# Kernel optimization log

Measured on AMD Instinct MI355X. Metric: run time of the kernel, lower is better.

The kernel has to match this reference:

```python
import jax, jax.numpy as jnp
import numpy as np

E = 2048          # embed_size
H = 32            # nums_head
KVH = 8           # nums_kv_head
D = E // H        # head_dim = 64
G = H // KVH      # group size = 4


def setup_inputs() -> dict:
    key = jax.random.key(0)
    ks = jax.random.split(key, 9)
    s = 0.02
    return {
        "datas": jax.random.normal(ks[0], (2, 2048, E), dtype=jnp.float32),
        "Wq": jax.random.normal(ks[1], (E, E), dtype=jnp.float32) * s,
        "bq": jnp.zeros((E,), dtype=jnp.float32),
        "Wk": jax.random.normal(ks[2], (E, KVH * D), dtype=jnp.float32) * s,
        "bk": jnp.zeros((KVH * D,), dtype=jnp.float32),
        "Wv": jax.random.normal(ks[3], (E, KVH * D), dtype=jnp.float32) * s,
        "bv": jnp.zeros((KVH * D,), dtype=jnp.float32),
        "Wo": jax.random.normal(ks[4], (E, E), dtype=jnp.float32) * s,
        "bo": jnp.zeros((E,), dtype=jnp.float32),
    }


def reference(datas, Wq, bq, Wk, bk, Wv, bv, Wo, bo):
    B, S, _ = datas.shape
    q = (datas @ Wq + bq).reshape(B, S, H, D).transpose(0, 2, 1, 3)    # [B,H,S,D]
    k = (datas @ Wk + bk).reshape(B, S, KVH, D).transpose(0, 2, 1, 3)  # [B,KVH,S,D]
    v = (datas @ Wv + bv).reshape(B, S, KVH, D).transpose(0, 2, 1, 3)
    # repeat_interleave along head dim: each kv head serves G consecutive q heads
    k = jnp.repeat(k, G, axis=1)  # [B,H,S,D]
    v = jnp.repeat(v, G, axis=1)
    scores = jnp.einsum("bhqd,bhkd->bhqk", q, k) / jnp.sqrt(jnp.asarray(D, q.dtype))
    attn = jax.nn.softmax(scores, axis=-1)  # dropout = identity (eval)
    out = jnp.einsum("bhqk,bhkd->bhqd", attn, v)       # [B,H,S,D]
    out = out.transpose(0, 2, 1, 3).reshape(B, S, E)   # [B,S,E]
    return out @ Wo + bo
```

## Files before the change

### kernel.cpp

```cpp
#include <hip/hip_runtime.h>
#include <hip/hip_bf16.h>
#include <stdint.h>


#define S_LEN 2048
#define EMB   2048
#define NH    32
#define NKVH  8
#define HD    64
#define MTOT  4096
#define NQKV  3072
#define KDIM  2048
#define QSCALE 0.18033688011112042f

typedef __attribute__((ext_vector_type(8))) short short8;
typedef __attribute__((ext_vector_type(4))) float f32x4;
typedef __attribute__((ext_vector_type(4))) unsigned int u32x4;
typedef unsigned int u32;

__device__ __forceinline__ unsigned short f2bf(float x) {
    unsigned int u = __builtin_bit_cast(unsigned int, x);
    u = (u + 0x7FFFu + ((u >> 16) & 1u)) >> 16;
    return (unsigned short)u;
}

__device__ __forceinline__ u32 cvtpk_bf16(float a, float b) {
    u32 r;
    asm("v_cvt_pk_bf16_f32 %0, %1, %2" : "=v"(r) : "v"(a), "v"(b));
    return r;
}

__device__ __forceinline__ float exp2_raw(float x) {
#if __has_builtin(__builtin_amdgcn_exp2f)
    return __builtin_amdgcn_exp2f(x);
#else
    float r;
    asm("v_exp_f32 %0, %1" : "=v"(r) : "v"(x));
    return r;
#endif
}

__device__ __forceinline__ float rcp_raw(float x) {
#if __has_builtin(__builtin_amdgcn_rcpf)
    return __builtin_amdgcn_rcpf(x);
#else
    float r;
    asm("v_rcp_f32 %0, %1" : "=v"(r) : "v"(x));
    return r;
#endif
}

#define GLOAD(src, dst)                                                                   \
    __builtin_amdgcn_global_load_lds((const __attribute__((address_space(1))) void*)(src),\
                                     (__attribute__((address_space(3))) void*)(dst), 16, 0, 0)

__global__ void cvt_x(const float* __restrict__ x, unsigned short* __restrict__ o, int n4) {
    int stride = gridDim.x * blockDim.x;
    for (int i = blockIdx.x * blockDim.x + threadIdx.x; i < n4; i += stride) {
        float4 v = ((const float4*)x)[i];
        ushort4 r;
        r.x = f2bf(v.x); r.y = f2bf(v.y); r.z = f2bf(v.z); r.w = f2bf(v.w);
        ((ushort4*)o)[i] = r;
    }
}

__global__ void transpose_all(const float* __restrict__ Wq, const float* __restrict__ Wk,
                              const float* __restrict__ Wv, const float* __restrict__ Wo,
                              const float* __restrict__ bq, const float* __restrict__ bk,
                              const float* __restrict__ bv,
                              unsigned short* __restrict__ Wqkvt, unsigned short* __restrict__ Wot,
                              float* __restrict__ biasq) {
    const int x = blockIdx.x;
    if (x == 80) {
        if (blockIdx.y == 0)
            for (int i = threadIdx.x; i < NQKV; i += 256) {
                if (i < EMB) biasq[i] = bq[i] * QSCALE;
                else if (i < EMB + 512) biasq[i] = bk[i - EMB];
                else biasq[i] = bv[i - EMB - 512];
            }
        return;
    }
    const float* src; unsigned short* dst; int N, rowOfs, nt; float scale;
    if (x < 32)      { src = Wq; dst = Wqkvt; N = 2048; rowOfs = 0;    nt = x;      scale = QSCALE; }
    else if (x < 40) { src = Wk; dst = Wqkvt; N = 512;  rowOfs = 2048; nt = x - 32; scale = 1.0f; }
    else if (x < 48) { src = Wv; dst = Wqkvt; N = 512;  rowOfs = 2560; nt = x - 40; scale = 1.0f; }
    else             { src = Wo; dst = Wot;   N = 2048; rowOfs = 0;    nt = x - 48; scale = 1.0f; }

    __shared__ float t[64][65];
    int n0 = nt * 64, k0 = blockIdx.y * 64;
    int c = threadIdx.x & 63, r0 = threadIdx.x >> 6;
    #pragma unroll
    for (int r = r0; r < 64; r += 4) t[r][c] = src[(size_t)(k0 + r) * N + n0 + c];
    __syncthreads();
    #pragma unroll
    for (int r = r0; r < 64; r += 4)
        dst[(size_t)(rowOfs + n0 + r) * KDIM + k0 + c] = f2bf(t[c][r] * scale);
}

__global__ void transpose_v(const unsigned short* __restrict__ qkv, unsigned short* __restrict__ vt) {
    __shared__ unsigned short t[64][72];
    int s0 = blockIdx.x * 64; int kvh = blockIdx.y; int b = blockIdx.z;
    int c = threadIdx.x & 63, r0 = threadIdx.x >> 6;
    #pragma unroll
    for (int r = r0; r < 64; r += 4)
        t[r][c] = qkv[(size_t)(b * S_LEN + s0 + r) * NQKV + (EMB + NKVH * HD) + kvh * HD + c];
    __syncthreads();
    #pragma unroll
    for (int r = r0; r < 64; r += 4)
        vt[(size_t)((b * NKVH + kvh) * HD + r) * S_LEN + s0 + c] = t[c][r];
}

template <bool OUT_BF16>
__global__ __launch_bounds__(256) void gemm_bt(const unsigned short* __restrict__ A,
                                               const unsigned short* __restrict__ Bt,
                                               const float* __restrict__ bias,
                                               void* __restrict__ Cout, int N) {
    __shared__ __align__(16) unsigned short As[128 * 32];
    __shared__ __align__(16) unsigned short Bs[128 * 32];
    const int t = threadIdx.x;
    const int lane = t & 63;
    const int l15 = lane & 15, hi = lane >> 4;
    const int w = t >> 6;
    const int wm = (w >> 1) * 64, wn = (w & 1) * 64;

    const unsigned nbx = gridDim.x;
    const unsigned flat = blockIdx.y * nbx + blockIdx.x;
    const unsigned cpx = (nbx * gridDim.y) >> 3;
    const unsigned swz = (flat & 7u) * cpx + (flat >> 3);
    const int m0 = (int)(swz / nbx) * 128, n0 = (int)(swz % nbx) * 128;

    const int srow = t >> 2, scol = (t & 3) * 8;
    const unsigned short* ag0 = A + (size_t)(m0 + srow) * KDIM + scol;
    const unsigned short* ag1 = ag0 + (size_t)64 * KDIM;
    const unsigned short* bg0 = Bt + (size_t)(n0 + srow) * KDIM + scol;
    const unsigned short* bg1 = bg0 + (size_t)64 * KDIM;

    f32x4 acc[4][4] = {};

    for (int k0 = 0; k0 < KDIM; k0 += 32) {
        GLOAD(ag0 + k0, As + t * 8);
        GLOAD(ag1 + k0, As + 2048 + t * 8);
        GLOAD(bg0 + k0, Bs + t * 8);
        GLOAD(bg1 + k0, Bs + 2048 + t * 8);
        __syncthreads();
        short8 af[4], bf[4];
        #pragma unroll
        for (int m = 0; m < 4; m++)
            af[m] = *(const short8*)(As + (wm + m * 16 + l15) * 32 + hi * 8);
        #pragma unroll
        for (int n = 0; n < 4; n++)
            bf[n] = *(const short8*)(Bs + (wn + n * 16 + l15) * 32 + hi * 8);
        __builtin_amdgcn_s_setprio(1);
        #pragma unroll
        for (int m = 0; m < 4; m++)
            #pragma unroll
            for (int n = 0; n < 4; n++)
                acc[m][n] = __builtin_amdgcn_mfma_f32_16x16x32_bf16(af[m], bf[n], acc[m][n], 0, 0, 0);
        __builtin_amdgcn_s_setprio(0);
        __syncthreads();
    }

    #pragma unroll
    for (int m = 0; m < 4; m++) {
        int row = m0 + wm + m * 16 + hi * 4;
        #pragma unroll
        for (int n = 0; n < 4; n++) {
            int col = n0 + wn + n * 16 + l15;
            float bb = bias[col];
            #pragma unroll
            for (int i = 0; i < 4; i++) {
                float v = acc[m][n][i] + bb;
                if (OUT_BF16) ((unsigned short*)Cout)[(size_t)(row + i) * N + col] = f2bf(v);
                else          ((float*)Cout)[(size_t)(row + i) * N + col] = v;
            }
        }
    }
}

__global__ __launch_bounds__(512, 4) void attn(const unsigned short* __restrict__ qkv,
                                               const unsigned short* __restrict__ vt,
                                               unsigned short* __restrict__ out) {
    constexpr int NT = S_LEN / 64;
    const int qt = blockIdx.x, h = blockIdx.y, b = blockIdx.z;
    const int kvh = h >> 2;
    const int t = threadIdx.x, lane = t & 63, w = t >> 6;
    const int l15 = lane & 15, hi = lane >> 4;
    const int xsw = l15 & 7;

    __shared__ __align__(16) unsigned short Ks[2][64 * 64];
    __shared__ __align__(16) unsigned short Vs[2][64 * 64];

    const int grpA = ((hi & 1) << 1) | (hi >> 1);
    const int laneA = l15 + grpA * 16;
    const int laneB = laneA ^ 16;
    const bool top = hi >= 2;

    u32x4 onesw;
    onesw[0] = 0x3F803F80u; onesw[1] = 0x3F803F80u; onesw[2] = 0x3F803F80u; onesw[3] = 0x3F803F80u;
    const short8 ones = __builtin_bit_cast(short8, onesw);
    const f32x4 fzero = {};

    const int qrow0 = b * S_LEN + qt * 256 + w * 32;
    short8 qf[2][2];
    #pragma unroll
    for (int nt = 0; nt < 2; nt++)
        #pragma unroll
        for (int ks = 0; ks < 2; ks++)
            qf[nt][ks] = *(const short8*)(qkv + (size_t)(qrow0 + nt * 16 + l15) * NQKV + h * HD + ks * 32 + hi * 8);

    f32x4 o[4][2] = {};
    f32x4 osum[2] = {};

    const unsigned short* kbase = qkv + (size_t)b * S_LEN * NQKV + EMB + kvh * HD;
    const unsigned short* vbase = vt + (size_t)(b * NKVH + kvh) * HD * S_LEN;

    const int sr = t >> 3;
    const int sc16 = ((t & 7) ^ (sr & 7)) * 8;
    const unsigned short* kg0 = kbase + (size_t)sr * NQKV + sc16;
    const unsigned short* vg0 = vbase + (size_t)sr * S_LEN + sc16;

#define STAGE(buf, kv0)                                               \
    do {                                                              \
        GLOAD(kg0 + (size_t)(kv0) * NQKV, &Ks[buf][t * 8]);           \
        GLOAD(vg0 + (kv0),                &Vs[buf][t * 8]);           \
    } while (0)

    STAGE(0, 0);
    __syncthreads();

    for (int tt = 0; tt < NT; tt++) {
        const int cur = tt & 1;
        if (tt + 1 < NT) STAGE(cur ^ 1, (tt + 1) * 64);

        const unsigned short* Kc = Ks[cur];
        const unsigned short* Vc = Vs[cur];

        f32x4 sc[4][2];
        {
            short8 kf[4];
            #pragma unroll
            for (int mt = 0; mt < 4; mt++)
                kf[mt] = *(const short8*)(Kc + (mt * 16 + l15) * 64 + ((hi ^ xsw) * 8));
            __builtin_amdgcn_s_setprio(1);
            #pragma unroll
            for (int mt = 0; mt < 4; mt++)
                #pragma unroll
                for (int nt = 0; nt < 2; nt++)
                    sc[mt][nt] = __builtin_amdgcn_mfma_f32_16x16x32_bf16(kf[mt], qf[nt][0], fzero, 0, 0, 0);
            __builtin_amdgcn_s_setprio(0);
        }
        {
            short8 kf[4];
            #pragma unroll
            for (int mt = 0; mt < 4; mt++)
                kf[mt] = *(const short8*)(Kc + (mt * 16 + l15) * 64 + (((4 + hi) ^ xsw) * 8));
            __builtin_amdgcn_s_setprio(1);
            #pragma unroll
            for (int mt = 0; mt < 4; mt++)
                #pragma unroll
                for (int nt = 0; nt < 2; nt++)
                    sc[mt][nt] = __builtin_amdgcn_mfma_f32_16x16x32_bf16(kf[mt], qf[nt][1], sc[mt][nt], 0, 0, 0);
            __builtin_amdgcn_s_setprio(0);
        }

        u32 w0[4][2], w1[4][2];
        #pragma unroll
        for (int nt = 0; nt < 2; nt++)
            #pragma unroll
            for (int mt = 0; mt < 4; mt++) {
                #pragma unroll
                for (int i = 0; i < 4; i++)
                    sc[mt][nt][i] = exp2_raw(sc[mt][nt][i]);
                w0[mt][nt] = cvtpk_bf16(sc[mt][nt][0], sc[mt][nt][1]);
                w1[mt][nt] = cvtpk_bf16(sc[mt][nt][2], sc[mt][nt][3]);
            }

        #pragma unroll
        for (int ks = 0; ks < 2; ks++) {
            short8 vf[4];
            #pragma unroll
            for (int dt = 0; dt < 4; dt++)
                vf[dt] = *(const short8*)(Vc + (dt * 16 + l15) * 64 + (((ks * 4 + hi) ^ xsw) * 8));
            #pragma unroll
            for (int nt = 0; nt < 2; nt++) {
                u32 a0 = (hi & 1) ? w0[2 * ks + 1][nt] : w0[2 * ks][nt];
                u32 a1 = (hi & 1) ? w1[2 * ks + 1][nt] : w1[2 * ks][nt];
                u32 b0 = (hi & 1) ? w0[2 * ks][nt] : w0[2 * ks + 1][nt];
                u32 b1 = (hi & 1) ? w1[2 * ks][nt] : w1[2 * ks + 1][nt];
                u32 r0 = (u32)__shfl((int)a0, laneA);
                u32 r1 = (u32)__shfl((int)a1, laneA);
                u32 r2 = (u32)__shfl((int)b0, laneB);
                u32 r3 = (u32)__shfl((int)b1, laneB);
                u32x4 pw;
                pw[0] = top ? r2 : r0;
                pw[1] = top ? r3 : r1;
                pw[2] = top ? r0 : r2;
                pw[3] = top ? r1 : r3;
                short8 pa = __builtin_bit_cast(short8, pw);
                __builtin_amdgcn_s_setprio(1);
                osum[nt] = __builtin_amdgcn_mfma_f32_16x16x32_bf16(ones, pa, osum[nt], 0, 0, 0);
                #pragma unroll
                for (int dt = 0; dt < 4; dt++)
                    o[dt][nt] = __builtin_amdgcn_mfma_f32_16x16x32_bf16(vf[dt], pa, o[dt][nt], 0, 0, 0);
                __builtin_amdgcn_s_setprio(0);
            }
        }
        __syncthreads();
    }
#undef STAGE

    #pragma unroll
    for (int nt = 0; nt < 2; nt++) {
        float inv = rcp_raw(osum[nt][0]);
        size_t rbase = (size_t)(qrow0 + nt * 16 + l15) * EMB + h * HD;
        #pragma unroll
        for (int dt = 0; dt < 4; dt++) {
            uint2 pk;
            pk.x = cvtpk_bf16(o[dt][nt][0] * inv, o[dt][nt][1] * inv);
            pk.y = cvtpk_bf16(o[dt][nt][2] * inv, o[dt][nt][3] * inv);
            *(uint2*)(out + rbase + dt * 16 + hi * 4) = pk;
        }
    }
}

extern "C" void kernel_launch(void* const* d_in, const int* in_sizes, int n_in,
                              void* d_out, int out_size, void* d_ws, size_t ws_size,
                              hipStream_t stream) {
    const float* datas = (const float*)d_in[0];
    const float* Wq = (const float*)d_in[1];
    const float* bq = (const float*)d_in[2];
    const float* Wk = (const float*)d_in[3];
    const float* bk = (const float*)d_in[4];
    const float* Wv = (const float*)d_in[5];
    const float* bv = (const float*)d_in[6];
    const float* Wo = (const float*)d_in[7];
    const float* bo = (const float*)d_in[8];
    float* out = (float*)d_out;

    char* ws = (char*)d_ws;
    unsigned short* Xb = (unsigned short*)ws;      ws += (size_t)MTOT * KDIM * 2;
    unsigned short* Wqkvt = (unsigned short*)ws;   ws += (size_t)NQKV * KDIM * 2;
    unsigned short* Wot = (unsigned short*)ws;     ws += (size_t)EMB * KDIM * 2;
    float* biasq = (float*)ws;                     ws += (size_t)NQKV * 4;
    unsigned short* QKV = (unsigned short*)ws;     ws += (size_t)MTOT * NQKV * 2;
    unsigned short* Vt = (unsigned short*)ws;      ws += (size_t)2 * NKVH * HD * S_LEN * 2;
    unsigned short* AO = (unsigned short*)ws;      ws += (size_t)MTOT * EMB * 2;

    cvt_x<<<2048, 256, 0, stream>>>(datas, Xb, MTOT * KDIM / 4);
    transpose_all<<<dim3(81, 32), 256, 0, stream>>>(Wq, Wk, Wv, Wo, bq, bk, bv,
                                                    Wqkvt, Wot, biasq);

    gemm_bt<true><<<dim3(NQKV / 128, MTOT / 128), 256, 0, stream>>>(Xb, Wqkvt, biasq, QKV, NQKV);
    transpose_v<<<dim3(S_LEN / 64, NKVH, 2), 256, 0, stream>>>(QKV, Vt);
    attn<<<dim3(S_LEN / 256, NH, 2), 512, 0, stream>>>(QKV, Vt, AO);
    gemm_bt<false><<<dim3(EMB / 128, MTOT / 128), 256, 0, stream>>>(AO, Wot, bo, out, EMB);
}
```

Measured before the change: 226.1 us.

## Double GEMM K-tile to 64 with XOR-swizzled LDS layout

The bf16 GEMM now stages a 128x64 K-slab per iteration instead of 128x32, halving the number of barrier pairs and loop iterations. The LDS rows are stored with an XOR swizzle of the 16-byte chunk index by row, and the fragment reads apply the same swizzle, to avoid LDS bank conflicts on the wider rows. LDS use per block doubles to 32 KB, which may reduce occupancy.

Measured after the change: 213.4 us. 5.6% less time.

```diff
diff --git a/kernel.cpp b/kernel.cpp
--- a/kernel.cpp
+++ b/kernel.cpp
@@ -115,11 +115,12 @@
                                                const unsigned short* __restrict__ Bt,
                                                const float* __restrict__ bias,
                                                void* __restrict__ Cout, int N) {
-    __shared__ __align__(16) unsigned short As[128 * 32];
-    __shared__ __align__(16) unsigned short Bs[128 * 32];
+    __shared__ __align__(16) unsigned short As[128 * 64];
+    __shared__ __align__(16) unsigned short Bs[128 * 64];
     const int t = threadIdx.x;
     const int lane = t & 63;
     const int l15 = lane & 15, hi = lane >> 4;
+    const int xsw = l15 & 7;
     const int w = t >> 6;
     const int wm = (w >> 1) * 64, wn = (w & 1) * 64;
 
@@ -129,34 +130,42 @@
     const unsigned swz = (flat & 7u) * cpx + (flat >> 3);
     const int m0 = (int)(swz / nbx) * 128, n0 = (int)(swz % nbx) * 128;
 
-    const int srow = t >> 2, scol = (t & 3) * 8;
-    const unsigned short* ag0 = A + (size_t)(m0 + srow) * KDIM + scol;
-    const unsigned short* ag1 = ag0 + (size_t)64 * KDIM;
-    const unsigned short* bg0 = Bt + (size_t)(n0 + srow) * KDIM + scol;
-    const unsigned short* bg1 = bg0 + (size_t)64 * KDIM;
+    const int srow = t >> 3;
+    const int scol = ((t & 7) ^ (srow & 7)) * 8;
+    const unsigned short* ag[4];
+    const unsigned short* bg[4];
+    #pragma unroll
+    for (int c = 0; c < 4; c++) {
+        ag[c] = A  + (size_t)(m0 + c * 32 + srow) * KDIM + scol;
+        bg[c] = Bt + (size_t)(n0 + c * 32 + srow) * KDIM + scol;
+    }
 
     f32x4 acc[4][4] = {};
 
-    for (int k0 = 0; k0 < KDIM; k0 += 32) {
-        GLOAD(ag0 + k0, As + t * 8);
-        GLOAD(ag1 + k0, As + 2048 + t * 8);
-        GLOAD(bg0 + k0, Bs + t * 8);
-        GLOAD(bg1 + k0, Bs + 2048 + t * 8);
+    for (int k0 = 0; k0 < KDIM; k0 += 64) {
+        #pragma unroll
+        for (int c = 0; c < 4; c++) {
+            GLOAD(ag[c] + k0, As + c * 2048 + t * 8);
+            GLOAD(bg[c] + k0, Bs + c * 2048 + t * 8);
+        }
         __syncthreads();
-        short8 af[4], bf[4];
-        #pragma unroll
-        for (int m = 0; m < 4; m++)
-            af[m] = *(const short8*)(As + (wm + m * 16 + l15) * 32 + hi * 8);
-        #pragma unroll
-        for (int n = 0; n < 4; n++)
-            bf[n] = *(const short8*)(Bs + (wn + n * 16 + l15) * 32 + hi * 8);
-        __builtin_amdgcn_s_setprio(1);
-        #pragma unroll
-        for (int m = 0; m < 4; m++)
+        #pragma unroll
+        for (int ks = 0; ks < 2; ks++) {
+            short8 af[4], bf[4];
+            #pragma unroll
+            for (int m = 0; m < 4; m++)
+                af[m] = *(const short8*)(As + (wm + m * 16 + l15) * 64 + (((ks * 4 + hi) ^ xsw) * 8));
             #pragma unroll
             for (int n = 0; n < 4; n++)
-                acc[m][n] = __builtin_amdgcn_mfma_f32_16x16x32_bf16(af[m], bf[n], acc[m][n], 0, 0, 0);
-        __builtin_amdgcn_s_setprio(0);
+                bf[n] = *(const short8*)(Bs + (wn + n * 16 + l15) * 64 + (((ks * 4 + hi) ^ xsw) * 8));
+            __builtin_amdgcn_s_setprio(1);
+            #pragma unroll
+            for (int m = 0; m < 4; m++)
+                #pragma unroll
+                for (int n = 0; n < 4; n++)
+                    acc[m][n] = __builtin_amdgcn_mfma_f32_16x16x32_bf16(af[m], bf[n], acc[m][n], 0, 0, 0);
+            __builtin_amdgcn_s_setprio(0);
+        }
         __syncthreads();
     }
 
```
